# Kernel tuning notes

Measured on AMD Instinct MI355X. Metric: run time of the kernel, lower is better.

## Reference

```python
import jax, jax.numpy as jnp
import numpy as np

B, S, H, N, D, R = 2, 2048, 768, 12, 64, 5  # batch, seq, hidden, heads, head_dim, n_structural_deps


def setup_inputs() -> dict:
    key = jax.random.key(0)
    ks = jax.random.split(key, 12)
    hidden_states = jax.random.normal(ks[0], (B, S, H), dtype=jnp.float32)
    attention_mask = jnp.zeros((B, 1, 1, S), dtype=jnp.float32)  # additive mask, all-visible
    # binary structural adjacency per dependency, broadcast over heads
    graph_adj = (jax.random.uniform(ks[1], (R, B, 1, S, S)) < 0.1).astype(jnp.float32)
    s = 0.02
    Wq = jax.random.normal(ks[2], (H, H), dtype=jnp.float32) * s
    bq = jnp.zeros((H,), dtype=jnp.float32)
    Wk = jax.random.normal(ks[3], (H, H), dtype=jnp.float32) * s
    bk = jnp.zeros((H,), dtype=jnp.float32)
    Wv = jax.random.normal(ks[4], (H, H), dtype=jnp.float32) * s
    bv = jnp.zeros((H,), dtype=jnp.float32)
    # biaffine bilinear forms, one [N, D, D] per structural dependency
    bili = jax.random.normal(ks[5], (R, N, D, D), dtype=jnp.float32) * s
    abs_bias = jnp.zeros((R, N), dtype=jnp.float32)  # initialized to zeros as in torch
    return {
        'hidden_states': hidden_states, 'attention_mask': attention_mask,
        'graph_adj': graph_adj, 'Wq': Wq, 'bq': bq, 'Wk': Wk, 'bk': bk,
        'Wv': Wv, 'bv': bv, 'bili': bili, 'abs_bias': abs_bias, 'layer_idx': 0,
    }


def reference(hidden_states, attention_mask, graph_adj, Wq, bq, Wk, bk, Wv, bv,
              bili, abs_bias, layer_idx):
    b, s, h = hidden_states.shape
    n, d = N, D

    def heads(x):  # [b, s, h] -> [b, n, s, d]
        return x.reshape(b, s, n, d).transpose(0, 2, 1, 3)

    q = heads(hidden_states @ Wq.T + bq)
    k = heads(hidden_states @ Wk.T + bk)
    v = heads(hidden_states @ Wv.T + bv)

    scores = jnp.einsum('bnid,bnjd->bnij', q, k)  # [b, n, s, s]
    # biaffine structural bias per dependency, masked by graph adjacency
    for i in range(R):  # small fixed structural loop
        bias = jnp.einsum('bnip,npq,bnjq->bnij', q, bili[i], k)
        bias = bias + abs_bias[i][None, :, None, None]
        scores = scores + bias * graph_adj[i]

    scores = scores / np.sqrt(d).astype(np.float32) + attention_mask
    probs = jax.nn.softmax(scores, axis=-1)
    ctx = jnp.einsum('bnij,bnjd->bnid', probs, v)  # [b, n, s, d]
    return ctx.transpose(0, 2, 1, 3).reshape(b, s, h)
```

## Files before the change

### kernel.cpp

```cpp
#include <hip/hip_runtime.h>
#include <cstdint>
#include <cstddef>

#define B_  2
#define S_  2048
#define H_  768
#define NH  12
#define DH  64
#define RD  5
#define BN  (B_*NH)

typedef _Float16 f16;
typedef __attribute__((ext_vector_type(8))) _Float16 f16x8;
typedef __attribute__((ext_vector_type(4))) float f32x4;

#define MFMA16(a, b, c) __builtin_amdgcn_mfma_f32_16x16x32_f16((a), (b), (c), 0, 0, 0)

#if __has_builtin(__builtin_amdgcn_exp2f)
__device__ __forceinline__ float exp2fast(float x) { return __builtin_amdgcn_exp2f(x); }
#else
__device__ __forceinline__ float exp2fast(float x) { return __expf(0.69314718056f * x); }
#endif

#define SCL 0.1803368801f
#define L2E 1.44269504f

#define NX4 ((B_*S_*H_)/4)
#define NW4 ((H_*H_)/4)

__global__ __launch_bounds__(256) void cvtall(
    const float* __restrict__ x,
    const float* __restrict__ wq, const float* __restrict__ wk,
    const float* __restrict__ wv,
    f16* __restrict__ xh, f16* __restrict__ wh)
{
    int idx = blockIdx.x * 256 + threadIdx.x;
    const int total4 = NX4 + 3 * NW4;
    if (idx >= total4) return;
    const float* src;
    f16* dst;
    int off;
    if (idx < NX4) {
        src = x; dst = xh; off = idx;
    } else {
        int r = idx - NX4;
        int which = r / NW4;
        off = r - which * NW4;
        src = (which == 0) ? wq : (which == 1) ? wk : wv;
        dst = wh + (size_t)which * H_ * H_;
    }
    float4 f = ((const float4*)src)[off];
    f16 h[4] = {(f16)f.x, (f16)f.y, (f16)f.z, (f16)f.w};
    ((ushort4*)dst)[off] = *(const ushort4*)h;
}

__global__ __launch_bounds__(256, 3) void qkv_gemm(
    const f16* __restrict__ xh, const f16* __restrict__ wh,
    const float* __restrict__ bq, const float* __restrict__ bk,
    const float* __restrict__ bv,
    f16* __restrict__ qo, f16* __restrict__ ko, f16* __restrict__ vt)
{
    __shared__ __align__(16) f16 Xs[64][72];
    __shared__ __align__(16) f16 Ws[3][64][72];

    const int tid = threadIdx.x;
    const int n  = blockIdx.x;
    const int m0 = blockIdx.y * 64;
    const int w = tid >> 6, lane = tid & 63;
    const int l15 = lane & 15, quad = lane >> 4;
    const int srow = tid >> 2, sc0 = (tid & 3) * 16;

    f32x4 acc[3][4];
#pragma unroll
    for (int i = 0; i < 3; ++i)
#pragma unroll
        for (int ns = 0; ns < 4; ++ns) acc[i][ns] = (f32x4){0.f, 0.f, 0.f, 0.f};

    const f16* xsrc = xh + (size_t)(m0 + srow) * H_ + sc0;
    const f16* wsrc = wh + (size_t)(n * 64 + srow) * H_ + sc0;

    for (int kc = 0; kc < 12; ++kc) {
        __syncthreads();
        {
            const f16* s0 = xsrc + kc * 64;
            *(f16x8*)&Xs[srow][sc0]     = *(const f16x8*)(s0);
            *(f16x8*)&Xs[srow][sc0 + 8] = *(const f16x8*)(s0 + 8);
        }
#pragma unroll
        for (int i = 0; i < 3; ++i) {
            const f16* s0 = wsrc + (size_t)i * H_ * H_ + kc * 64;
            *(f16x8*)&Ws[i][srow][sc0]     = *(const f16x8*)(s0);
            *(f16x8*)&Ws[i][srow][sc0 + 8] = *(const f16x8*)(s0 + 8);
        }
        __syncthreads();

        f16x8 a0 = *(const f16x8*)&Xs[w * 16 + l15][quad * 8];
        f16x8 a1 = *(const f16x8*)&Xs[w * 16 + l15][quad * 8 + 32];
#pragma unroll
        for (int i = 0; i < 3; ++i)
#pragma unroll
            for (int ns = 0; ns < 4; ++ns) {
                f16x8 b0 = *(const f16x8*)&Ws[i][ns * 16 + l15][quad * 8];
                f16x8 b1 = *(const f16x8*)&Ws[i][ns * 16 + l15][quad * 8 + 32];
                acc[i][ns] = MFMA16(a0, b0, acc[i][ns]);
                acc[i][ns] = MFMA16(a1, b1, acc[i][ns]);
            }
    }
    __syncthreads();

    const float* bias[3] = {bq, bk, bv};
    f16 (*T0)[72] = Xs;
    f16 (*T1)[72] = Ws[0];
    f16 (*T2)[72] = Ws[1];
#pragma unroll
    for (int i = 0; i < 3; ++i) {
        f16 (*T)[72] = (i == 0) ? T0 : (i == 1) ? T1 : T2;
#pragma unroll
        for (int ns = 0; ns < 4; ++ns) {
            float bb = bias[i][n * 64 + ns * 16 + l15];
#pragma unroll
            for (int reg = 0; reg < 4; ++reg)
                T[w * 16 + quad * 4 + reg][ns * 16 + l15] =
                    (f16)(acc[i][ns][reg] + bb);
        }
    }
    __syncthreads();

    const int mrow = m0 + srow;
    const int bb2 = mrow >> 11, ss = mrow & 2047;
    {
        f16* dst = qo + ((size_t)(bb2 * NH + n) * S_ + ss) * DH + sc0;
        *(f16x8*)dst       = *(const f16x8*)&T0[srow][sc0];
        *(f16x8*)(dst + 8) = *(const f16x8*)&T0[srow][sc0 + 8];
    }
    {
        f16* dst = ko + ((size_t)(bb2 * NH + n) * S_ + ss) * DH + sc0;
        *(f16x8*)dst       = *(const f16x8*)&T1[srow][sc0];
        *(f16x8*)(dst + 8) = *(const f16x8*)&T1[srow][sc0 + 8];
    }
    {
        f16 tmp[16];
#pragma unroll
        for (int u = 0; u < 16; ++u) tmp[u] = T2[sc0 + u][srow];
        f16* dst = vt + ((size_t)(bb2 * NH + n) * DH + srow) * S_ + (m0 & 2047) + sc0;
        *(f16x8*)dst       = *(const f16x8*)&tmp[0];
        *(f16x8*)(dst + 8) = *(const f16x8*)&tmp[8];
    }
}

__global__ __launch_bounds__(256) void adjpack(
    const float* __restrict__ adj, unsigned char* __restrict__ adjp)
{
    const int idx4 = blockIdx.x * 256 + threadIdx.x;
    const int j4 = idx4 & 511;
    const int iq = (idx4 >> 9) & 511;
    const int b  = idx4 >> 18;
    unsigned int wbits[4] = {0, 0, 0, 0};
#pragma unroll
    for (int r = 0; r < RD; ++r) {
#pragma unroll
        for (int ii = 0; ii < 4; ++ii) {
            float4 v = *(const float4*)(adj +
                (((size_t)(r * B_ + b) * S_) + iq * 4 + ii) * S_ + j4 * 4);
            float vv[4] = {v.x, v.y, v.z, v.w};
#pragma unroll
            for (int jj = 0; jj < 4; ++jj)
                wbits[jj] |= (vv[jj] != 0.f ? 1u : 0u) << (r + 8 * ii);
        }
    }
    uint4 pk = {wbits[0], wbits[1], wbits[2], wbits[3]};
    *(uint4*)(adjp + ((size_t)(b * 512 + iq) * S_ + j4 * 4) * 4) = pk;
}

__global__ __launch_bounds__(256, 3) void attn(
    const f16* __restrict__ q, const f16* __restrict__ k, const f16* __restrict__ vt,
    const float* __restrict__ bili, const unsigned char* __restrict__ adjp,
    const float* __restrict__ mask, const float* __restrict__ absb,
    float* __restrict__ po, float* __restrict__ pm, float* __restrict__ pl)
{
    __shared__ __align__(16) char smem[9216 + 9216 + 128];
    f16*   Mt  = (f16*)smem;
    f16*   Pb  = (f16*)(smem + 9216);
    float* lut = (float*)(smem + 9216 + 9216);

    const int tid = threadIdx.x;
    const int idx = blockIdx.x;
    const int g = idx & 7;
    const int it = (idx >> 3) & 31;
    const int half = (idx >> 8) & 1;
    const int bn = 8 * (idx >> 9) + g;
    const int b = bn / NH, n = bn % NH;
    const int w = tid >> 6, lane = tid & 63;
    const int l15 = lane & 15, quad = lane >> 4;
    const int wi0 = it * 64 + w * 16;
    const size_t kbase = (size_t)bn * S_ * DH;

    if (tid < 32) {
        float a = 0.f;
#pragma unroll
        for (int r = 0; r < RD; ++r)
            if (tid & (1 << r)) a += absb[r * NH + n];
        lut[tid] = a * SCL;
    }

    const f16* qrow = q + kbase + (size_t)(wi0 + l15) * DH + quad * 8;
    f16x8 aq0 = *(const f16x8*)(qrow);
    f16x8 aq1 = *(const f16x8*)(qrow + 32);

    f16* Pw = Pb + w * 16 * 72;

    f16x8 aqp[RD][2];
#pragma unroll 1
    for (int r = 0; r < RD; ++r) {
        __syncthreads();
        {
            int p = tid >> 2, q0 = (tid & 3) * 16;
            const float* src = bili + ((size_t)(r * NH + n) * DH + p) * DH + q0;
            float4 g0 = ((const float4*)src)[0];
            float4 g1 = ((const float4*)src)[1];
            float4 g2 = ((const float4*)src)[2];
            float4 g3 = ((const float4*)src)[3];
            float mv[16] = {g0.x, g0.y, g0.z, g0.w, g1.x, g1.y, g1.z, g1.w,
                            g2.x, g2.y, g2.z, g2.w, g3.x, g3.y, g3.z, g3.w};
#pragma unroll
            for (int u = 0; u < 16; ++u) Mt[(q0 + u) * 72 + p] = (f16)mv[u];
        }
        __syncthreads();
#pragma unroll
        for (int ns = 0; ns < 4; ++ns) {
            f16x8 b0 = *(const f16x8*)&Mt[(ns * 16 + l15) * 72 + quad * 8];
            f16x8 b1 = *(const f16x8*)&Mt[(ns * 16 + l15) * 72 + quad * 8 + 32];
            f32x4 d = {0.f, 0.f, 0.f, 0.f};
            d = MFMA16(aq0, b0, d);
            d = MFMA16(aq1, b1, d);
#pragma unroll
            for (int reg = 0; reg < 4; ++reg)
                Pw[(quad * 4 + reg) * 72 + ns * 16 + l15] = (f16)d[reg];
        }
        aqp[r][0] = *(const f16x8*)&Pw[l15 * 72 + quad * 8];
        aqp[r][1] = *(const f16x8*)&Pw[l15 * 72 + quad * 8 + 32];
    }

    f16x8 ones;
#pragma unroll
    for (int u = 0; u < 8; ++u) ones[u] = (f16)1.0f;

    f32x4 o[4] = {{0,0,0,0},{0,0,0,0},{0,0,0,0},{0,0,0,0}};
    f32x4 lacc = {0.f, 0.f, 0.f, 0.f};
    float mrun[4] = {-1e30f, -1e30f, -1e30f, -1e30f};

    const unsigned char* adjrow =
        adjp + (size_t)(b * 512 + (wi0 >> 2) + quad) * (S_ * 4);
    const float* maskrow = mask + (size_t)b * S_;
    const f16* vtb = vt + (size_t)bn * DH * S_;

    const int t0 = half * 16;
    for (int t = t0; t < t0 + 16; ++t) {
        const int j0 = t * 64;
        float sc[4][4];

#pragma unroll
        for (int js = 0; js < 4; ++js) {
            const int jcol = j0 + js * 16 + l15;
            const f16* kp = k + kbase + (size_t)jcol * DH + quad * 8;
            f16x8 bk0 = *(const f16x8*)(kp);
            f16x8 bk1 = *(const f16x8*)(kp + 32);

            f32x4 aqk = {0.f, 0.f, 0.f, 0.f};
            aqk = MFMA16(aq0, bk0, aqk);
            aqk = MFMA16(aq1, bk1, aqk);
            f32x4 ar[RD];
#pragma unroll
            for (int r = 0; r < RD; ++r) {
                f32x4 z = {0.f, 0.f, 0.f, 0.f};
                z = MFMA16(aqp[r][0], bk0, z);
                z = MFMA16(aqp[r][1], bk1, z);
                ar[r] = z;
            }

            uchar4 a4 = *(const uchar4*)(adjrow + (size_t)jcol * 4);
            unsigned int bbits[4] = {a4.x, a4.y, a4.z, a4.w};
            float mkL = maskrow[jcol] * L2E;
#pragma unroll
            for (int reg = 0; reg < 4; ++reg) {
                float s = aqk[reg];
                unsigned int bt = bbits[reg];
#pragma unroll
                for (int r = 0; r < RD; ++r)
                    s = fmaf((float)((bt >> r) & 1u), ar[r][reg], s);
                sc[js][reg] = fmaf(s, SCL, lut[bt] + mkL);
            }
        }

        float alpha[4];
#pragma unroll
        for (int reg = 0; reg < 4; ++reg) {
            float nm = fmaxf(fmaxf(sc[0][reg], sc[1][reg]),
                             fmaxf(sc[2][reg], sc[3][reg]));
#pragma unroll
            for (int off = 1; off < 16; off <<= 1)
                nm = fmaxf(nm, __shfl_xor(nm, off));
            float mn = fmaxf(mrun[reg], nm);
            alpha[reg] = exp2fast(mrun[reg] - mn);
            mrun[reg] = mn;
        }
#pragma unroll
        for (int js = 0; js < 4; ++js)
#pragma unroll
            for (int reg = 0; reg < 4; ++reg) {
                float p = exp2fast(sc[js][reg] - mrun[reg]);
                Pw[(quad * 4 + reg) * 72 + js * 16 + l15] = (f16)p;
            }
#pragma unroll
        for (int reg = 0; reg < 4; ++reg) {
            lacc[reg] *= alpha[reg];
#pragma unroll
            for (int ds = 0; ds < 4; ++ds) o[ds][reg] *= alpha[reg];
        }

        f16x8 pa0 = *(const f16x8*)&Pw[l15 * 72 + quad * 8];
        f16x8 pa1 = *(const f16x8*)&Pw[l15 * 72 + quad * 8 + 32];
        lacc = MFMA16(pa0, ones, lacc);
        lacc = MFMA16(pa1, ones, lacc);
#pragma unroll
        for (int ds = 0; ds < 4; ++ds) {
            const f16* vp = vtb + (size_t)(ds * 16 + l15) * S_ + j0 + quad * 8;
            f16x8 bv0 = *(const f16x8*)(vp);
            f16x8 bv1 = *(const f16x8*)(vp + 32);
            o[ds] = MFMA16(pa0, bv0, o[ds]);
            o[ds] = MFMA16(pa1, bv1, o[ds]);
        }
    }

    const size_t rbase = (size_t)(half * BN + bn) * S_;
#pragma unroll
    for (int reg = 0; reg < 4; ++reg) {
        int i = wi0 + quad * 4 + reg;
        float* prow = po + (rbase + i) * 64;
#pragma unroll
        for (int ds = 0; ds < 4; ++ds)
            prow[ds * 16 + l15] = o[ds][reg];
        if (l15 == 0) {
            pm[rbase + i] = mrun[reg];
            pl[rbase + i] = lacc[reg];
        }
    }
}

__global__ __launch_bounds__(256) void merge(
    const float* __restrict__ po, const float* __restrict__ pm,
    const float* __restrict__ pl, float* __restrict__ out)
{
    const int t = blockIdx.x * 256 + threadIdx.x;
    const int rid = t >> 4;
    const int d4 = t & 15;
    const int bn = rid >> 11, row = rid & 2047;
    const int b = bn / NH, n = bn % NH;

    const float m0 = pm[rid], m1 = pm[BN * S_ + rid];
    const float l0 = pl[rid], l1 = pl[BN * S_ + rid];
    const float mN = fmaxf(m0, m1);
    const float c0 = exp2fast(m0 - mN), c1 = exp2fast(m1 - mN);
    const float inv = 1.f / (l0 * c0 + l1 * c1);

    const float4 o0 = ((const float4*)po)[(size_t)rid * 16 + d4];
    const float4 o1 = ((const float4*)po)[((size_t)BN * S_ + rid) * 16 + d4];
    float4 r;
    r.x = (o0.x * c0 + o1.x * c1) * inv;
    r.y = (o0.y * c0 + o1.y * c1) * inv;
    r.z = (o0.z * c0 + o1.z * c1) * inv;
    r.w = (o0.w * c0 + o1.w * c1) * inv;
    ((float4*)out)[(size_t)(b * S_ + row) * (H_ / 4) + n * (DH / 4) + d4] = r;
}

extern "C" void kernel_launch(void* const* d_in, const int* in_sizes, int n_in,
                              void* d_out, int out_size, void* d_ws, size_t ws_size,
                              hipStream_t stream)
{
    const float* hs   = (const float*)d_in[0];
    const float* mask = (const float*)d_in[1];
    const float* adj  = (const float*)d_in[2];
    const float* Wq   = (const float*)d_in[3];
    const float* bq   = (const float*)d_in[4];
    const float* Wk   = (const float*)d_in[5];
    const float* bk   = (const float*)d_in[6];
    const float* Wv   = (const float*)d_in[7];
    const float* bv   = (const float*)d_in[8];
    const float* bili = (const float*)d_in[9];
    const float* absb = (const float*)d_in[10];
    float* out = (float*)d_out;

    const size_t QKV = (size_t)BN * S_ * DH;
    f16* q  = (f16*)d_ws;
    f16* k  = q + QKV;
    f16* vt = k + QKV;
    unsigned char* adjp = (unsigned char*)(vt + QKV);
    f16* xh = (f16*)(adjp + (size_t)B_ * 512 * S_ * 4);
    f16* wh = xh + (size_t)B_ * S_ * H_;
    float* po = (float*)(wh + (size_t)3 * H_ * H_);
    float* pm = po + (size_t)2 * BN * S_ * DH;
    float* pl = pm + (size_t)2 * BN * S_;

    const int total4 = NX4 + 3 * NW4;
    cvtall<<<(total4 + 255) / 256, 256, 0, stream>>>(hs, Wq, Wk, Wv, xh, wh);
    qkv_gemm<<<dim3(12, 64), 256, 0, stream>>>(xh, wh, bq, bk, bv, q, k, vt);
    adjpack<<<2048, 256, 0, stream>>>(adj, adjp);
    attn<<<1536, 256, 0, stream>>>(q, k, vt, bili, adjp, mask, absb, po, pm, pl);
    merge<<<3072, 256, 0, stream>>>(po, pm, pl, out);
}
```

Before: 564.0 us.

## Fuse fp16 conversion and adjacency packing into QKV GEMM, precompute q' projections

Removes the separate fp32-to-fp16 conversion kernel by converting X and W tiles on the fly inside the QKV GEMM. The adjacency bit-packing runs as extra blocks of the same launch. The per-dependency q·bili projections move from the attention prologue into a separate qprime kernel that writes them to global memory. Attention drops its Mt shared buffer, raises its occupancy hint to 4, and interleaves each biaffine MFMA with its masked FMA to lower register pressure. The trade-off is fewer launches and a lighter attention prologue against extra global traffic for the stored q' tensors and redundant weight conversion across GEMM blocks.

```diff
diff --git a/kernel.cpp b/kernel.cpp
--- a/kernel.cpp
+++ b/kernel.cpp
@@ -25,47 +25,59 @@
 #define SCL 0.1803368801f
 #define L2E 1.44269504f
 
-#define NX4 ((B_*S_*H_)/4)
-#define NW4 ((H_*H_)/4)
-
-__global__ __launch_bounds__(256) void cvtall(
-    const float* __restrict__ x,
-    const float* __restrict__ wq, const float* __restrict__ wk,
-    const float* __restrict__ wv,
-    f16* __restrict__ xh, f16* __restrict__ wh)
-{
-    int idx = blockIdx.x * 256 + threadIdx.x;
-    const int total4 = NX4 + 3 * NW4;
-    if (idx >= total4) return;
-    const float* src;
-    f16* dst;
-    int off;
-    if (idx < NX4) {
-        src = x; dst = xh; off = idx;
-    } else {
-        int r = idx - NX4;
-        int which = r / NW4;
-        off = r - which * NW4;
-        src = (which == 0) ? wq : (which == 1) ? wk : wv;
-        dst = wh + (size_t)which * H_ * H_;
-    }
-    float4 f = ((const float4*)src)[off];
-    f16 h[4] = {(f16)f.x, (f16)f.y, (f16)f.z, (f16)f.w};
-    ((ushort4*)dst)[off] = *(const ushort4*)h;
-}
-
-__global__ __launch_bounds__(256, 3) void qkv_gemm(
-    const f16* __restrict__ xh, const f16* __restrict__ wh,
+__device__ __forceinline__ void cvt16(const float* __restrict__ src, f16* dst)
+{
+    float4 f0 = ((const float4*)src)[0];
+    float4 f1 = ((const float4*)src)[1];
+    float4 f2 = ((const float4*)src)[2];
+    float4 f3 = ((const float4*)src)[3];
+    f16 h[16] = {(f16)f0.x, (f16)f0.y, (f16)f0.z, (f16)f0.w,
+                 (f16)f1.x, (f16)f1.y, (f16)f1.z, (f16)f1.w,
+                 (f16)f2.x, (f16)f2.y, (f16)f2.z, (f16)f2.w,
+                 (f16)f3.x, (f16)f3.y, (f16)f3.z, (f16)f3.w};
+    *(f16x8*)dst       = *(const f16x8*)&h[0];
+    *(f16x8*)(dst + 8) = *(const f16x8*)&h[8];
+}
+
+__global__ __launch_bounds__(256, 3) void qkv_pack(
+    const float* __restrict__ hs,
+    const float* __restrict__ Wq, const float* __restrict__ Wk,
+    const float* __restrict__ Wv,
     const float* __restrict__ bq, const float* __restrict__ bk,
     const float* __restrict__ bv,
-    f16* __restrict__ qo, f16* __restrict__ ko, f16* __restrict__ vt)
+    f16* __restrict__ qo, f16* __restrict__ ko, f16* __restrict__ vt,
+    const float* __restrict__ adj, unsigned char* __restrict__ adjp)
 {
     __shared__ __align__(16) f16 Xs[64][72];
     __shared__ __align__(16) f16 Ws[3][64][72];
 
     const int tid = threadIdx.x;
-    const int n  = blockIdx.x;
-    const int m0 = blockIdx.y * 64;
+
+    if (blockIdx.x >= 768) {
+        const int idx4 = (blockIdx.x - 768) * 256 + tid;
+        const int j4 = idx4 & 511;
+        const int iq = (idx4 >> 9) & 511;
+        const int b  = idx4 >> 18;
+        unsigned int wbits[4] = {0, 0, 0, 0};
+#pragma unroll
+        for (int r = 0; r < RD; ++r) {
+#pragma unroll
+            for (int ii = 0; ii < 4; ++ii) {
+                float4 v = *(const float4*)(adj +
+                    (((size_t)(r * B_ + b) * S_) + iq * 4 + ii) * S_ + j4 * 4);
+                float vv[4] = {v.x, v.y, v.z, v.w};
+#pragma unroll
+                for (int jj = 0; jj < 4; ++jj)
+                    wbits[jj] |= (vv[jj] != 0.f ? 1u : 0u) << (r + 8 * ii);
+            }
+        }
+        uint4 pk = {wbits[0], wbits[1], wbits[2], wbits[3]};
+        *(uint4*)(adjp + ((size_t)(b * 512 + iq) * S_ + j4 * 4) * 4) = pk;
+        return;
+    }
+
+    const int n  = blockIdx.x % 12;
+    const int m0 = (blockIdx.x / 12) * 64;
     const int w = tid >> 6, lane = tid & 63;
     const int l15 = lane & 15, quad = lane >> 4;
     const int srow = tid >> 2, sc0 = (tid & 3) * 16;
@@ -76,22 +88,17 @@
 #pragma unroll
         for (int ns = 0; ns < 4; ++ns) acc[i][ns] = (f32x4){0.f, 0.f, 0.f, 0.f};
 
-    const f16* xsrc = xh + (size_t)(m0 + srow) * H_ + sc0;
-    const f16* wsrc = wh + (size_t)(n * 64 + srow) * H_ + sc0;
+    const float* xsrc = hs + (size_t)(m0 + srow) * H_ + sc0;
+    const float* w0src = Wq + (size_t)(n * 64 + srow) * H_ + sc0;
+    const float* w1src = Wk + (size_t)(n * 64 + srow) * H_ + sc0;
+    const float* w2src = Wv + (size_t)(n * 64 + srow) * H_ + sc0;
 
     for (int kc = 0; kc < 12; ++kc) {
         __syncthreads();
-        {
-            const f16* s0 = xsrc + kc * 64;
-            *(f16x8*)&Xs[srow][sc0]     = *(const f16x8*)(s0);
-            *(f16x8*)&Xs[srow][sc0 + 8] = *(const f16x8*)(s0 + 8);
-        }
-#pragma unroll
-        for (int i = 0; i < 3; ++i) {
-            const f16* s0 = wsrc + (size_t)i * H_ * H_ + kc * 64;
-            *(f16x8*)&Ws[i][srow][sc0]     = *(const f16x8*)(s0);
-            *(f16x8*)&Ws[i][srow][sc0 + 8] = *(const f16x8*)(s0 + 8);
-        }
+        cvt16(xsrc  + kc * 64, &Xs[srow][sc0]);
+        cvt16(w0src + kc * 64, &Ws[0][srow][sc0]);
+        cvt16(w1src + kc * 64, &Ws[1][srow][sc0]);
+        cvt16(w2src + kc * 64, &Ws[2][srow][sc0]);
         __syncthreads();
 
         f16x8 a0 = *(const f16x8*)&Xs[w * 16 + l15][quad * 8];
@@ -148,40 +155,73 @@
     }
 }
 
-__global__ __launch_bounds__(256) void adjpack(
-    const float* __restrict__ adj, unsigned char* __restrict__ adjp)
-{
-    const int idx4 = blockIdx.x * 256 + threadIdx.x;
-    const int j4 = idx4 & 511;
-    const int iq = (idx4 >> 9) & 511;
-    const int b  = idx4 >> 18;
-    unsigned int wbits[4] = {0, 0, 0, 0};
+__global__ __launch_bounds__(256, 3) void qprime(
+    const f16* __restrict__ q, const float* __restrict__ bili,
+    f16* __restrict__ qp)
+{
+    __shared__ __align__(16) f16 Mt[64 * 72];
+    __shared__ __align__(16) f16 Pb[4 * 16 * 72];
+
+    const int tid = threadIdx.x;
+    const int idx = blockIdx.x;
+    const int it = idx & 31;
+    const int bn = idx >> 5;
+    const int n = bn % NH;
+    const int w = tid >> 6, lane = tid & 63;
+    const int l15 = lane & 15, quad = lane >> 4;
+    const int wi0 = it * 64 + w * 16;
+    const size_t kbase = (size_t)bn * S_ * DH;
+
+    const f16* qrow = q + kbase + (size_t)(wi0 + l15) * DH + quad * 8;
+    f16x8 aq0 = *(const f16x8*)(qrow);
+    f16x8 aq1 = *(const f16x8*)(qrow + 32);
+
+    f16* Pw = Pb + w * 16 * 72;
+
 #pragma unroll
     for (int r = 0; r < RD; ++r) {
-#pragma unroll
-        for (int ii = 0; ii < 4; ++ii) {
-            float4 v = *(const float4*)(adj +
-                (((size_t)(r * B_ + b) * S_) + iq * 4 + ii) * S_ + j4 * 4);
-            float vv[4] = {v.x, v.y, v.z, v.w};
-#pragma unroll
-            for (int jj = 0; jj < 4; ++jj)
-                wbits[jj] |= (vv[jj] != 0.f ? 1u : 0u) << (r + 8 * ii);
-        }
-    }
-    uint4 pk = {wbits[0], wbits[1], wbits[2], wbits[3]};
-    *(uint4*)(adjp + ((size_t)(b * 512 + iq) * S_ + j4 * 4) * 4) = pk;
-}
-
-__global__ __launch_bounds__(256, 3) void attn(
+        __syncthreads();
+        {
+            int p = tid >> 2, q0 = (tid & 3) * 16;
+            const float* src = bili + ((size_t)(r * NH + n) * DH + p) * DH + q0;
+            float4 g0 = ((const float4*)src)[0];
+            float4 g1 = ((const float4*)src)[1];
+            float4 g2 = ((const float4*)src)[2];
+            float4 g3 = ((const float4*)src)[3];
+            float mv[16] = {g0.x, g0.y, g0.z, g0.w, g1.x, g1.y, g1.z, g1.w,
+                            g2.x, g2.y, g2.z, g2.w, g3.x, g3.y, g3.z, g3.w};
+#pragma unroll
+            for (int u = 0; u < 16; ++u) Mt[(q0 + u) * 72 + p] = (f16)mv[u];
+        }
+        __syncthreads();
+#pragma unroll
+        for (int ns = 0; ns < 4; ++ns) {
+            f16x8 b0 = *(const f16x8*)&Mt[(ns * 16 + l15) * 72 + quad * 8];
+            f16x8 b1 = *(const f16x8*)&Mt[(ns * 16 + l15) * 72 + quad * 8 + 32];
+            f32x4 d = {0.f, 0.f, 0.f, 0.f};
+            d = MFMA16(aq0, b0, d);
+            d = MFMA16(aq1, b1, d);
+#pragma unroll
+            for (int reg = 0; reg < 4; ++reg)
+                Pw[(quad * 4 + reg) * 72 + ns * 16 + l15] = (f16)d[reg];
+        }
+        f16x8 v0 = *(const f16x8*)&Pw[l15 * 72 + quad * 8];
+        f16x8 v1 = *(const f16x8*)&Pw[l15 * 72 + quad * 8 + 32];
+        f16* dst = qp + ((size_t)(bn * RD + r) * S_ + wi0 + l15) * 64 + quad * 8;
+        *(f16x8*)dst        = v0;
+        *(f16x8*)(dst + 32) = v1;
+    }
+}
+
+__global__ __launch_bounds__(256, 4) void attn(
     const f16* __restrict__ q, const f16* __restrict__ k, const f16* __restrict__ vt,
-    const float* __restrict__ bili, const unsigned char* __restrict__ adjp,
+    const f16* __restrict__ qp, const unsigned char* __restrict__ adjp,
     const float* __restrict__ mask, const float* __restrict__ absb,
     float* __restrict__ po, float* __restrict__ pm, float* __restrict__ pl)
 {
-    __shared__ __align__(16) char smem[9216 + 9216 + 128];
-    f16*   Mt  = (f16*)smem;
-    f16*   Pb  = (f16*)(smem + 9216);
-    float* lut = (float*)(smem + 9216 + 9216);
+    __shared__ __align__(16) char smem[9216 + 128];
+    f16*   Pb  = (f16*)smem;
+    float* lut = (float*)(smem + 9216);
 
     const int tid = threadIdx.x;
     const int idx = blockIdx.x;
@@ -202,44 +242,23 @@
             if (tid & (1 << r)) a += absb[r * NH + n];
         lut[tid] = a * SCL;
     }
+    __syncthreads();
 
     const f16* qrow = q + kbase + (size_t)(wi0 + l15) * DH + quad * 8;
     f16x8 aq0 = *(const f16x8*)(qrow);
     f16x8 aq1 = *(const f16x8*)(qrow + 32);
 
+    f16x8 aqp[RD][2];
+    {
+        const f16* qpb = qp + ((size_t)(bn * RD) * S_ + wi0 + l15) * 64 + quad * 8;
+#pragma unroll
+        for (int r = 0; r < RD; ++r) {
+            aqp[r][0] = *(const f16x8*)(qpb + (size_t)r * S_ * 64);
+            aqp[r][1] = *(const f16x8*)(qpb + (size_t)r * S_ * 64 + 32);
+        }
+    }
+
     f16* Pw = Pb + w * 16 * 72;
-
-    f16x8 aqp[RD][2];
-#pragma unroll 1
-    for (int r = 0; r < RD; ++r) {
-        __syncthreads();
-        {
-            int p = tid >> 2, q0 = (tid & 3) * 16;
-            const float* src = bili + ((size_t)(r * NH + n) * DH + p) * DH + q0;
-            float4 g0 = ((const float4*)src)[0];
-            float4 g1 = ((const float4*)src)[1];
-            float4 g2 = ((const float4*)src)[2];
-            float4 g3 = ((const float4*)src)[3];
-            float mv[16] = {g0.x, g0.y, g0.z, g0.w, g1.x, g1.y, g1.z, g1.w,
-                            g2.x, g2.y, g2.z, g2.w, g3.x, g3.y, g3.z, g3.w};
-#pragma unroll
-            for (int u = 0; u < 16; ++u) Mt[(q0 + u) * 72 + p] = (f16)mv[u];
-        }
-        __syncthreads();
-#pragma unroll
-        for (int ns = 0; ns < 4; ++ns) {
-            f16x8 b0 = *(const f16x8*)&Mt[(ns * 16 + l15) * 72 + quad * 8];
-            f16x8 b1 = *(const f16x8*)&Mt[(ns * 16 + l15) * 72 + quad * 8 + 32];
-            f32x4 d = {0.f, 0.f, 0.f, 0.f};
-            d = MFMA16(aq0, b0, d);
-            d = MFMA16(aq1, b1, d);
-#pragma unroll
-            for (int reg = 0; reg < 4; ++reg)
-                Pw[(quad * 4 + reg) * 72 + ns * 16 + l15] = (f16)d[reg];
-        }
-        aqp[r][0] = *(const f16x8*)&Pw[l15 * 72 + quad * 8];
-        aqp[r][1] = *(const f16x8*)&Pw[l15 * 72 + quad * 8 + 32];
-    }
 
     f16x8 ones;
 #pragma unroll
@@ -255,6 +274,7 @@
     const f16* vtb = vt + (size_t)bn * DH * S_;
 
     const int t0 = half * 16;
+#pragma unroll 1
     for (int t = t0; t < t0 + 16; ++t) {
         const int j0 = t * 64;
         float sc[4][4];
@@ -269,27 +289,26 @@
             f32x4 aqk = {0.f, 0.f, 0.f, 0.f};
             aqk = MFMA16(aq0, bk0, aqk);
             aqk = MFMA16(aq1, bk1, aqk);
-            f32x4 ar[RD];
+
+            uchar4 a4 = *(const uchar4*)(adjrow + (size_t)jcol * 4);
+            unsigned int bbits[4] = {a4.x, a4.y, a4.z, a4.w};
+            float mkL = maskrow[jcol] * L2E;
+
+            float s0 = aqk[0], s1 = aqk[1], s2 = aqk[2], s3 = aqk[3];
 #pragma unroll
             for (int r = 0; r < RD; ++r) {
                 f32x4 z = {0.f, 0.f, 0.f, 0.f};
                 z = MFMA16(aqp[r][0], bk0, z);
                 z = MFMA16(aqp[r][1], bk1, z);
-                ar[r] = z;
+                s0 = fmaf((float)((bbits[0] >> r) & 1u), z[0], s0);
+                s1 = fmaf((float)((bbits[1] >> r) & 1u), z[1], s1);
+                s2 = fmaf((float)((bbits[2] >> r) & 1u), z[2], s2);
+                s3 = fmaf((float)((bbits[3] >> r) & 1u), z[3], s3);
             }
-
-            uchar4 a4 = *(const uchar4*)(adjrow + (size_t)jcol * 4);
-            unsigned int bbits[4] = {a4.x, a4.y, a4.z, a4.w};
-            float mkL = maskrow[jcol] * L2E;
-#pragma unroll
-            for (int reg = 0; reg < 4; ++reg) {
-                float s = aqk[reg];
-                unsigned int bt = bbits[reg];
-#pragma unroll
-                for (int r = 0; r < RD; ++r)
-                    s = fmaf((float)((bt >> r) & 1u), ar[r][reg], s);
-                sc[js][reg] = fmaf(s, SCL, lut[bt] + mkL);
-            }
+            sc[js][0] = fmaf(s0, SCL, lut[bbits[0]] + mkL);
+            sc[js][1] = fmaf(s1, SCL, lut[bbits[1]] + mkL);
+            sc[js][2] = fmaf(s2, SCL, lut[bbits[2]] + mkL);
+            sc[js][3] = fmaf(s3, SCL, lut[bbits[3]] + mkL);
         }
 
         float alpha[4];
@@ -395,16 +414,14 @@
     f16* k  = q + QKV;
     f16* vt = k + QKV;
     unsigned char* adjp = (unsigned char*)(vt + QKV);
-    f16* xh = (f16*)(adjp + (size_t)B_ * 512 * S_ * 4);
-    f16* wh = xh + (size_t)B_ * S_ * H_;
-    float* po = (float*)(wh + (size_t)3 * H_ * H_);
+    f16* qp = (f16*)(adjp + (size_t)B_ * 512 * S_ * 4);
+    float* po = (float*)(qp + (size_t)RD * QKV);
     float* pm = po + (size_t)2 * BN * S_ * DH;
     float* pl = pm + (size_t)2 * BN * S_;
 
-    const int total4 = NX4 + 3 * NW4;
-    cvtall<<<(total4 + 255) / 256, 256, 0, stream>>>(hs, Wq, Wk, Wv, xh, wh);
-    qkv_gemm<<<dim3(12, 64), 256, 0, stream>>>(xh, wh, bq, bk, bv, q, k, vt);
-    adjpack<<<2048, 256, 0, stream>>>(adj, adjp);
-    attn<<<1536, 256, 0, stream>>>(q, k, vt, bili, adjp, mask, absb, po, pm, pl);
+    qkv_pack<<<768 + 2048, 256, 0, stream>>>(hs, Wq, Wk, Wv, bq, bk, bv,
+                                             q, k, vt, adj, adjp);
+    qprime<<<768, 256, 0, stream>>>(q, bili, qp);
+    attn<<<1536, 256, 0, stream>>>(q, k, vt, qp, adjp, mask, absb, po, pm, pl);
     merge<<<3072, 256, 0, stream>>>(po, pm, pl, out);
 }
```

Result: no change. 572.7 us (+1.5%).
